# Performance work log

Measured on AMD Instinct MI355X. Metric: run time of the kernel, lower is better.

The kernel has to match this reference:

```python
import jax, jax.numpy as jnp
import numpy as np

B, N, D = 4, 2048, 1024
H, S, C, NSH, MV = 8, 3, 32, 3, 4


def _lin(key, fan_in, fan_out):
    k1, k2 = jax.random.split(key)
    lim = 1.0 / np.sqrt(fan_in)
    W = jax.random.uniform(k1, (fan_in, fan_out), minval=-lim, maxval=lim)
    b = jax.random.uniform(k2, (fan_out,), minval=-lim, maxval=lim)
    return W, b


def setup_inputs() -> dict:
    key = jax.random.key(0)
    ks = jax.random.split(key, 16)
    x = jax.random.normal(ks[0], (B, N, D), dtype=jnp.float32)
    W_sense, b_sense = _lin(ks[1], D, S * D)
    W_ctx, b_ctx = _lin(ks[2], D, D)
    W_sel, b_sel = _lin(ks[3], 2 * D, S)
    W_charge, b_charge = _lin(ks[4], D, 1)
    W_shell, b_shell = _lin(ks[5], D, NSH)
    W_class, b_class = _lin(ks[6], D, C)
    W_mass, b_mass = _lin(ks[7], D, 1)
    W_val, b_val = _lin(ks[8], D, MV)
    sparsity = 0.4
    init_val = -np.log(1.0 / sparsity - 1.0)
    compat_logits = jax.random.normal(ks[9], (C, C)) * 0.5 + init_val
    W_v, b_v = _lin(ks[10], D, D)
    W_out, b_out = _lin(ks[11], D, D)
    return {
        'x': x,
        'W_sense': W_sense, 'b_sense': b_sense,
        'W_ctx': W_ctx, 'b_ctx': b_ctx,
        'W_sel': W_sel, 'b_sel': b_sel,
        'W_charge': W_charge, 'b_charge': b_charge,
        'W_shell': W_shell, 'b_shell': b_shell,
        'W_class': W_class, 'b_class': b_class,
        'W_mass': W_mass, 'b_mass': b_mass,
        'W_val': W_val, 'b_val': b_val,
        'compat_logits': compat_logits.astype(jnp.float32),
        'w_charge': jnp.float32(1.0), 'w_shell': jnp.float32(0.5),
        'w_distance': jnp.float32(1.0), 'w_mass': jnp.float32(0.3),
        'w_valence': jnp.float32(0.3), 'temperature': jnp.float32(1.0),
        'W_v': W_v, 'b_v': b_v,
        'W_out': W_out, 'b_out': b_out,
    }


def reference(x, W_sense, b_sense, W_ctx, b_ctx, W_sel, b_sel,
              W_charge, b_charge, W_shell, b_shell, W_class, b_class,
              W_mass, b_mass, W_val, b_val, compat_logits,
              w_charge, w_shell, w_distance, w_mass, w_valence, temperature,
              W_v, b_v, W_out, b_out):
    b, n, d = x.shape
    sp = jax.nn.softplus

    # --- isotope selection (word-sense mixing) ---
    senses = (x @ W_sense + b_sense).reshape(b, n, S, d)          # (B,N,S,D)
    ctx_avg = (x @ W_ctx + b_ctx).mean(axis=1, keepdims=True)     # (B,1,D)
    sel_in = jnp.concatenate([x, jnp.broadcast_to(ctx_avg, (b, n, d))], axis=-1)
    sense_w = jax.nn.softmax(sel_in @ W_sel + b_sel, axis=-1)     # (B,N,S)
    x = jnp.einsum('bns,bnsd->bnd', sense_w, senses)

    # --- atomic properties ---
    charge = jnp.tanh(x @ W_charge + b_charge)[..., 0]            # (B,N)
    shell = jax.nn.softmax(x @ W_shell + b_shell, axis=-1)        # (B,N,NSH)
    cls = jnp.argmax(x @ W_class + b_class, axis=-1)              # (B,N) int
    mass = sp(x @ W_mass + b_mass)[..., 0] + 0.5                  # (B,N)
    val = jax.nn.softmax(x @ W_val + b_val, axis=-1)              # (B,N,MV)

    # --- class compatibility mask (B,N,N) ---
    compat = jax.nn.sigmoid((compat_logits + compat_logits.T) * 0.5)
    sparse_mask = compat[cls[:, :, None], cls[:, None, :]]

    # --- pairwise physics energy (B,N,N) ---
    pos = jnp.arange(n, dtype=x.dtype)
    dist = jnp.abs(pos[:, None] - pos[None, :])                   # (N,N)
    val_sum = val.sum(axis=-1)                                    # (B,N)
    E = (sp(w_charge) * charge[:, :, None] * charge[:, None, :]
         + sp(w_shell) * jnp.abs(shell[:, :, None, :] - shell[:, None, :, :]).sum(-1)
         - sp(w_distance) / (1.0 + 0.1 * dist)
         + sp(w_mass) * 0.1 * mass[:, :, None] * mass[:, None, :]
         - sp(w_valence) * (val_sum[:, :, None] + val_sum[:, None, :]) * 0.5)

    temp = sp(temperature)
    scores = (-E / temp) * sparse_mask
    causal = jnp.triu(jnp.ones((n, n), dtype=bool), k=1)
    scores = jnp.where(causal[None], -jnp.inf, scores)
    attn = jax.nn.softmax(scores, axis=-1)                        # (B,N,N)

    # --- weighted value aggregation (shared attn across heads) ---
    V = (x @ W_v + b_v).reshape(b, n, H, d // H)
    out = jnp.einsum('bij,bjhd->bihd', attn, V).reshape(b, n, d)
    return out @ W_out + b_out
```

## Files before the change

kernel.cpp:

```cpp
#include <hip/hip_runtime.h>
#include <hip/hip_bf16.h>
#include <cmath>

typedef __hip_bfloat16 bf16;
typedef __attribute__((ext_vector_type(4))) float floatx4;
typedef __attribute__((ext_vector_type(8))) short short8;
typedef __attribute__((ext_vector_type(8))) unsigned short ushort8;

__device__ __forceinline__ float bf2f(bf16 v) { return __bfloat162float(v); }
__device__ __forceinline__ bf16 f2bf(float v) { return __float2bfloat16(v); }
__device__ __forceinline__ float bfu2f(unsigned short u) { return __uint_as_float(((unsigned)u) << 16); }
__device__ __forceinline__ unsigned short f2bfu(float v) {
  bf16 h = __float2bfloat16(v);
  return __builtin_bit_cast(unsigned short, h);
}
__device__ __forceinline__ float softplusf(float x) {
  return x > 20.0f ? x : log1pf(expf(x));
}

__device__ __forceinline__ void async16(const void* g, void* l) {
  __builtin_amdgcn_global_load_lds(
      (const __attribute__((address_space(1))) unsigned int*)g,
      (__attribute__((address_space(3))) unsigned int*)l, 16, 0, 0);
}

template<int MODE, int CAUSAL, int ACCUM, int SWZ, int KSPLIT = 1>
__global__ __launch_bounds__(256) void gemm_bt(
    const bf16* __restrict__ A, const bf16* __restrict__ Bt,
    const float* __restrict__ bias, void* __restrict__ Cptr,
    int M, int N, int K, int lda, int ldb, int ldc,
    long aoffz, long boffz, long coffz)
{
  __shared__ __align__(16) bf16 As[128 * 32];
  __shared__ __align__(16) bf16 Bs[128 * 32];

  const int tid = threadIdx.x;
  const int lane = tid & 63;
  const int wave = tid >> 6;
  const int wr = wave >> 1, wc = wave & 1;
  const long z = blockIdx.z;
  int kstart = 0;
  long zz = z;
  if (KSPLIT > 1) {
    kstart = (int)(z % KSPLIT) * K;
    zz = z / KSPLIT;
  }
  A += zz * aoffz;
  Bt += zz * boffz;

  int bx, by;
  if (SWZ) {
    const int mtiles = M >> 7;
    const int per = mtiles >> 3;
    const int bid = (int)blockIdx.x;
    const int xcd = bid & 7;
    const int slot = bid >> 3;
    by = xcd * per + (slot % per);
    bx = slot / per;
  } else {
    bx = blockIdx.x;
    by = blockIdx.y;
  }
  const int m0 = by * 128, n0 = bx * 128;
  int kend = kstart + K;
  if (CAUSAL) {
    int klim = (by + 1) * 128;
    if (klim < kend) kend = klim;
  }

  floatx4 acc[4][4] = {};

  const int c0 = tid, c1 = tid + 256;
  const int ar0 = c0 >> 2, ak0 = (c0 & 3) * 8;
  const int ar1 = c1 >> 2, ak1 = (c1 & 3) * 8;
  const int fm = lane & 15, fk = (lane >> 4) * 8;

  for (int k0 = kstart; k0 < kend; k0 += 32) {
    async16(&A[(size_t)(m0 + ar0) * lda + k0 + ak0], &As[c0 * 8]);
    async16(&A[(size_t)(m0 + ar1) * lda + k0 + ak1], &As[c1 * 8]);
    async16(&Bt[(size_t)(n0 + ar0) * ldb + k0 + ak0], &Bs[c0 * 8]);
    async16(&Bt[(size_t)(n0 + ar1) * ldb + k0 + ak1], &Bs[c1 * 8]);
    __syncthreads();

    short8 af[4], bfr[4];
#pragma unroll
    for (int i = 0; i < 4; i++)
      af[i] = *(const short8*)&As[(wr * 64 + i * 16 + fm) * 32 + fk];
#pragma unroll
    for (int j = 0; j < 4; j++)
      bfr[j] = *(const short8*)&Bs[(wc * 64 + j * 16 + fm) * 32 + fk];
#pragma unroll
    for (int i = 0; i < 4; i++)
#pragma unroll
      for (int j = 0; j < 4; j++)
        acc[i][j] = __builtin_amdgcn_mfma_f32_16x16x32_bf16(af[i], bfr[j], acc[i][j], 0, 0, 0);
    __syncthreads();
  }

  const int rm0 = (lane >> 4) * 4, cn = lane & 15;
#pragma unroll
  for (int i = 0; i < 4; i++) {
#pragma unroll
    for (int j = 0; j < 4; j++) {
      int nn = n0 + wc * 64 + j * 16 + cn;
      float bv = bias ? bias[nn] : 0.0f;
#pragma unroll
      for (int r = 0; r < 4; r++) {
        int mm = m0 + wr * 64 + i * 16 + rm0 + r;
        float v = acc[i][j][r] + bv;
        if (MODE == 0) {
          ((bf16*)Cptr)[z * coffz + (long)mm * ldc + nn] = f2bf(v);
        } else if (MODE == 1) {
          long idx = z * coffz + (long)mm * ldc + nn;
          float* Cf = (float*)Cptr;
          if (ACCUM) v += Cf[idx];
          Cf[idx] = v;
        } else {
          long idx = ((long)((mm >> 11) * 1024 + nn)) * 2048 + (mm & 2047);
          ((bf16*)Cptr)[idx] = f2bf(v);
        }
      }
    }
  }
}

__global__ __launch_bounds__(256) void gemm_sense(
    const bf16* __restrict__ A, const bf16* __restrict__ Bt,
    const float* __restrict__ bias, const float* __restrict__ sw,
    bf16* __restrict__ y)
{
  __shared__ __align__(16) bf16 As[128 * 32];
  __shared__ __align__(16) bf16 Bs[128 * 32];

  const int tid = threadIdx.x;
  const int lane = tid & 63;
  const int wave = tid >> 6;
  const int wr = wave >> 1, wc = wave & 1;

  const int bid = (int)blockIdx.x;
  const int xcd = bid & 7;
  const int slot = bid >> 3;
  const int by = xcd * 8 + (slot & 7);
  const int bx = slot >> 3;
  const int m0 = by * 128, n0 = bx * 128;

  const int c0 = tid, c1 = tid + 256;
  const int ar0 = c0 >> 2, ak0 = (c0 & 3) * 8;
  const int ar1 = c1 >> 2, ak1 = (c1 & 3) * 8;
  const int fm = lane & 15, fk = (lane >> 4) * 8;
  const int rm0 = (lane >> 4) * 4, cn = lane & 15;

  floatx4 yacc[4][4] = {};

#pragma unroll 1
  for (int s = 0; s < 3; s++) {
    floatx4 acc[4][4] = {};
    const bf16* Bsrc = Bt + (size_t)(s * 1024 + n0) * 1024;
    for (int k0 = 0; k0 < 1024; k0 += 32) {
      async16(&A[(size_t)(m0 + ar0) * 3072 + k0 + ak0], &As[c0 * 8]);
      async16(&A[(size_t)(m0 + ar1) * 3072 + k0 + ak1], &As[c1 * 8]);
      async16(&Bsrc[(size_t)ar0 * 1024 + k0 + ak0], &Bs[c0 * 8]);
      async16(&Bsrc[(size_t)ar1 * 1024 + k0 + ak1], &Bs[c1 * 8]);
      __syncthreads();

      short8 af[4], bfr[4];
#pragma unroll
      for (int i = 0; i < 4; i++)
        af[i] = *(const short8*)&As[(wr * 64 + i * 16 + fm) * 32 + fk];
#pragma unroll
      for (int j = 0; j < 4; j++)
        bfr[j] = *(const short8*)&Bs[(wc * 64 + j * 16 + fm) * 32 + fk];
#pragma unroll
      for (int i = 0; i < 4; i++)
#pragma unroll
        for (int j = 0; j < 4; j++)
          acc[i][j] = __builtin_amdgcn_mfma_f32_16x16x32_bf16(af[i], bfr[j], acc[i][j], 0, 0, 0);
      __syncthreads();
    }
    float swm[4][4];
#pragma unroll
    for (int i = 0; i < 4; i++)
#pragma unroll
      for (int r = 0; r < 4; r++)
        swm[i][r] = sw[(size_t)(m0 + wr * 64 + i * 16 + rm0 + r) * 4 + s];
#pragma unroll
    for (int j = 0; j < 4; j++) {
      int nn = n0 + wc * 64 + j * 16 + cn;
      float bv = bias[s * 1024 + nn];
#pragma unroll
      for (int i = 0; i < 4; i++)
#pragma unroll
        for (int r = 0; r < 4; r++)
          yacc[i][j][r] += swm[i][r] * (acc[i][j][r] + bv);
    }
  }

#pragma unroll
  for (int i = 0; i < 4; i++)
#pragma unroll
    for (int j = 0; j < 4; j++) {
      int nn = n0 + wc * 64 + j * 16 + cn;
#pragma unroll
      for (int r = 0; r < 4; r++) {
        int mm = m0 + wr * 64 + i * 16 + rm0 + r;
        y[(size_t)mm * 1024 + nn] = f2bf(yacc[i][j][r]);
      }
    }
}

__global__ __launch_bounds__(256) void k_split_x3(const float* __restrict__ x,
                                                  bf16* __restrict__ xhhl) {
  long id = (long)blockIdx.x * 256 + threadIdx.x;
  if (id >= 8388608L) return;
  long t = id >> 10;
  int d = (int)(id & 1023);
  float v = x[id];
  bf16 h = f2bf(v);
  bf16 l = f2bf(v - bf2f(h));
  bf16* row = xhhl + t * 3072;
  row[d] = h;
  row[1024 + d] = h;
  row[2048 + d] = l;
}

__global__ __launch_bounds__(256) void k_split_ws3(const float* __restrict__ Ws,
                                                   bf16* __restrict__ Wsn3) {
  long id = (long)blockIdx.x * 256 + threadIdx.x;
  if (id >= 3145728L) return;
  int row10 = (int)(id >> 10);
  int d = row10 / 3;
  int s = row10 - d * 3;
  int dp = (int)(id & 1023);
  float v = Ws[id];
  bf16 h = f2bf(v);
  bf16 l = f2bf(v - bf2f(h));
  bf16* row = Wsn3 + ((size_t)(s * 1024 + d)) * 3072;
  row[dp] = h;
  row[1024 + dp] = l;
  row[2048 + dp] = h;
}

__global__ __launch_bounds__(256) void k_trans_hl(const float* __restrict__ src,
                                                  bf16* __restrict__ dh,
                                                  int R, int C) {
  __shared__ float tile[32][33];
  int c0 = blockIdx.x * 32, r0 = blockIdx.y * 32;
  int tx = threadIdx.x & 31, ty = threadIdx.x >> 5;
  for (int rr = ty; rr < 32; rr += 8)
    tile[rr][tx] = src[(size_t)(r0 + rr) * C + c0 + tx];
  __syncthreads();
  for (int rr = ty; rr < 32; rr += 8)
    dh[(size_t)(c0 + rr) * R + r0 + tx] = f2bf(tile[tx][rr]);
}

__global__ __launch_bounds__(256) void k_pack(
    const float* __restrict__ W_charge, const float* __restrict__ W_shell,
    const float* __restrict__ W_class, const float* __restrict__ W_mass,
    const float* __restrict__ b_charge, const float* __restrict__ b_shell,
    const float* __restrict__ b_class, const float* __restrict__ b_mass,
    const float* __restrict__ compat_logits,
    bf16* __restrict__ Whhl3, float* __restrict__ bhead, float* __restrict__ csig)
{
  int c = blockIdx.x;
  int tid = threadIdx.x;
  for (int e = tid; e < 1024; e += 256) {
    float v;
    if (c == 0) v = W_charge[e];
    else if (c < 4) v = W_shell[e * 3 + (c - 1)];
    else if (c == 4) v = W_mass[e];
    else if (c < 37) v = W_class[e * 32 + (c - 5)];
    else v = 0.0f;
    bf16 h = f2bf(v);
    bf16 l = f2bf(v - bf2f(h));
    bf16* row = Whhl3 + (size_t)c * 3072;
    row[e] = h;
    row[1024 + e] = h;
    row[2048 + e] = l;
  }
  if (c == 0 && tid < 37) {
    float v;
    if (tid == 0) v = b_charge[0];
    else if (tid < 4) v = b_shell[tid - 1];
    else if (tid == 4) v = b_mass[0];
    else v = b_class[tid - 5];
    bhead[tid] = v;
  }
  if (c == 1) {
    for (int k = tid; k < 1024; k += 256) {
      int ii = k >> 5, jj = k & 31;
      float l = 0.5f * (compat_logits[ii * 32 + jj] + compat_logits[jj * 32 + ii]);
      csig[k] = 1.0f / (1.0f + expf(-l));
    }
  }
}

__global__ __launch_bounds__(256) void k_bh(
    const float* __restrict__ b_sense, const float* __restrict__ W_charge,
    const float* __restrict__ W_shell, const float* __restrict__ W_class,
    const float* __restrict__ W_mass, float* __restrict__ bh)
{
  const int c = blockIdx.x, s = blockIdx.y;
  const int tid = threadIdx.x;
  __shared__ float red[256];
  float p = 0.0f;
  for (int e = tid; e < 1024; e += 256) {
    float w;
    if (c == 0) w = W_charge[e];
    else if (c < 4) w = W_shell[e * 3 + (c - 1)];
    else if (c == 4) w = W_mass[e];
    else w = W_class[e * 32 + (c - 5)];
    p += b_sense[s * 1024 + e] * w;
  }
  red[tid] = p;
  __syncthreads();
  for (int st = 128; st > 0; st >>= 1) {
    if (tid < st) red[tid] += red[tid + st];
    __syncthreads();
  }
  if (tid == 0) bh[s * 128 + c] = red[0];
}

__global__ __launch_bounds__(256) void k_reduce_mt(const float* __restrict__ Mtp,
                                                   float* __restrict__ Mt) {
  long o = (long)blockIdx.x * 256 + threadIdx.x;
  if (o >= 393216L) return;
  long s = o >> 17;
  long i = o & 131071;
  const float* p = Mtp + s * 8 * 131072 + i;
  float acc = 0.0f;
#pragma unroll
  for (int kc = 0; kc < 8; kc++) acc += p[(size_t)kc * 131072];
  Mt[o] = acc;
}

__global__ __launch_bounds__(256) void k_split(const float* __restrict__ Mt,
                                               const float* __restrict__ W_sel,
                                               bf16* __restrict__ Mthl) {
  long id = (long)blockIdx.x * 256 + threadIdx.x;
  if (id >= 1572864L) return;
  int n = (int)(id / 3072);
  int k = (int)(id - (long)n * 3072);
  int third = k >> 10;
  int j = k & 1023;
  float v;
  if (n < 384) {
    v = Mt[(size_t)n * 1024 + j];
  } else {
    int c2 = n - 384;
    v = (c2 < 3) ? W_sel[(size_t)j * 3 + c2] : 0.0f;
  }
  bf16 h = f2bf(v);
  Mthl[id] = (third == 1) ? f2bf(v - bf2f(h)) : h;
}

__global__ __launch_bounds__(256) void k_xbar(const float* __restrict__ x, float* __restrict__ xbar) {
  const int d = blockIdx.x * 256 + threadIdx.x;
  const int b = blockIdx.y;
  const int n0 = blockIdx.z * 256;
  const float* xb = x + (size_t)b * 2048 * 1024 + (size_t)n0 * 1024 + d;
  float s = 0.0f;
  for (int n = 0; n < 256; n++) s += xb[(size_t)n * 1024];
  atomicAdd(&xbar[b * 1024 + d], s * (1.0f / 2048.0f));
}

__global__ __launch_bounds__(256) void k_q(const float* __restrict__ W_ctx,
                                           const float* __restrict__ b_ctx,
                                           const float* __restrict__ W_sel,
                                           float* __restrict__ q) {
  const int e = blockIdx.x;
  const int tid = threadIdx.x;
  const float* row = (e < 1024) ? (W_ctx + (size_t)e * 1024) : b_ctx;
  float p0 = 0.0f, p1 = 0.0f, p2 = 0.0f;
  for (int d = tid; d < 1024; d += 256) {
    float v = row[d];
    const float* ws = W_sel + (size_t)(1024 + d) * 3;
    p0 += v * ws[0]; p1 += v * ws[1]; p2 += v * ws[2];
  }
  __shared__ float red[3][256];
  red[0][tid] = p0; red[1][tid] = p1; red[2][tid] = p2;
  __syncthreads();
  for (int st = 128; st > 0; st >>= 1) {
    if (tid < st) {
      red[0][tid] += red[0][tid + st];
      red[1][tid] += red[1][tid + st];
      red[2][tid] += red[2][tid + st];
    }
    __syncthreads();
  }
  if (tid < 3) q[(size_t)e * 3 + tid] = red[tid][0];
}

__global__ __launch_bounds__(256) void k_ctxsel(const float* __restrict__ xbar,
                                                const float* __restrict__ q,
                                                float* __restrict__ ctx_sel) {
  const int b = blockIdx.x;
  const int tid = threadIdx.x;
  float p0 = 0.0f, p1 = 0.0f, p2 = 0.0f;
  for (int e = tid; e < 1024; e += 256) {
    float v = xbar[b * 1024 + e];
    p0 += v * q[e * 3 + 0]; p1 += v * q[e * 3 + 1]; p2 += v * q[e * 3 + 2];
  }
  __shared__ float red[3][256];
  red[0][tid] = p0; red[1][tid] = p1; red[2][tid] = p2;
  __syncthreads();
  for (int st = 128; st > 0; st >>= 1) {
    if (tid < st) {
      red[0][tid] += red[0][tid + st];
      red[1][tid] += red[1][tid + st];
      red[2][tid] += red[2][tid + st];
    }
    __syncthreads();
  }
  if (tid < 3) ctx_sel[b * 3 + tid] = red[tid][0] + q[1024 * 3 + tid];
}

__global__ __launch_bounds__(64) void k_heads(
    const float* __restrict__ H, const float* __restrict__ ctx_sel,
    const float* __restrict__ b_sel, const float* __restrict__ bh,
    const float* __restrict__ bhead,
    float* __restrict__ sw, float* __restrict__ feat)
{
  const int t = blockIdx.x;
  const int b = t >> 11;
  const int lane = threadIdx.x;
  const float* Ht = H + (size_t)t * 512;
  const float* Ht2 = H + 4194304 + (size_t)t * 512;

  float s0 = Ht[384] + Ht2[384] + ctx_sel[b * 3 + 0] + b_sel[0];
  float s1 = Ht[385] + Ht2[385] + ctx_sel[b * 3 + 1] + b_sel[1];
  float s2 = Ht[386] + Ht2[386] + ctx_sel[b * 3 + 2] + b_sel[2];
  float mx = fmaxf(s0, fmaxf(s1, s2));
  float e0 = expf(s0 - mx), e1 = expf(s1 - mx), e2 = expf(s2 - mx);
  float inv = 1.0f / (e0 + e1 + e2);
  float w0 = e0 * inv, w1 = e1 * inv, w2 = e2 * inv;

  __shared__ float L[64];
  if (lane < 37) {
    float lg = bhead[lane];
    lg += w0 * (Ht[lane] + Ht2[lane] + bh[lane]);
    lg += w1 * (Ht[128 + lane] + Ht2[128 + lane] + bh[128 + lane]);
    lg += w2 * (Ht[256 + lane] + Ht2[256 + lane] + bh[256 + lane]);
    L[lane] = lg;
  }
  __syncthreads();
  if (lane == 0) {
    float charge = tanhf(L[0]);
    float h0 = L[1], h1 = L[2], h2 = L[3];
    float hm = fmaxf(h0, fmaxf(h1, h2));
    float x0 = expf(h0 - hm), x1 = expf(h1 - hm), x2 = expf(h2 - hm);
    float hinv = 1.0f / (x0 + x1 + x2);
    float mass = softplusf(L[4]) + 0.5f;
    int cls = 0;
    float best = L[5];
    for (int c = 1; c < 32; c++) {
      if (L[5 + c] > best) { best = L[5 + c]; cls = c; }
    }
    float* f = feat + (size_t)t * 8;
    f[0] = charge; f[1] = mass;
    f[2] = x0 * hinv; f[3] = x1 * hinv; f[4] = x2 * hinv;
    f[5] = (float)cls; f[6] = 0.0f; f[7] = 0.0f;
    float* sp_ = sw + (size_t)t * 4;
    sp_[0] = w0; sp_[1] = w1; sp_[2] = w2; sp_[3] = 0.0f;
  }
}

__global__ __launch_bounds__(256) void k_scores(
    const float* __restrict__ feat, const float* __restrict__ compat,
    const float* __restrict__ wchg, const float* __restrict__ wsh,
    const float* __restrict__ wdist, const float* __restrict__ wmass,
    const float* __restrict__ wval, const float* __restrict__ temp_p,
    bf16* __restrict__ P)
{
  const int i = blockIdx.x, b = blockIdx.y;
  const int tid = threadIdx.x;
  __shared__ float cs[1024];
  __shared__ float red[256];
  for (int k = tid; k < 1024; k += 256) cs[k] = compat[k];
  __syncthreads();

  const float a = softplusf(wchg[0]);
  const float bs = softplusf(wsh[0]);
  const float c = softplusf(wdist[0]);
  const float dm = softplusf(wmass[0]);
  const float ev = softplusf(wval[0]);
  const float itmp = 1.0f / softplusf(temp_p[0]);

  const float4* fi4 = (const float4*)(feat + ((size_t)b * 2048 + i) * 8);
  float4 fiA = fi4[0], fiB = fi4[1];
  const float ci = fiA.x, mi = fiA.y, si0 = fiA.z, si1 = fiA.w, si2 = fiB.x;
  int cli = (int)fiB.y; cli = cli < 0 ? 0 : (cli > 31 ? 31 : cli);

  float sc[8];
  float lmax = -3.0e38f;
#pragma unroll
  for (int jj = 0; jj < 8; jj++) {
    int j = tid + jj * 256;
    const float4* fj4 = (const float4*)(feat + ((size_t)b * 2048 + j) * 8);
    float4 fjA = fj4[0], fjB = fj4[1];
    int clj = (int)fjB.y; clj = clj < 0 ? 0 : (clj > 31 ? 31 : clj);
    float E = a * ci * fjA.x
            + bs * (fabsf(si0 - fjA.z) + fabsf(si1 - fjA.w) + fabsf(si2 - fjB.x))
            - c / (1.0f + 0.1f * fabsf((float)(i - j)))
            + dm * 0.1f * mi * fjA.y
            - ev;
    float s = (j <= i) ? (-E * itmp) * cs[cli * 32 + clj] : -3.0e38f;
    sc[jj] = s;
    lmax = fmaxf(lmax, s);
  }
  red[tid] = lmax;
  __syncthreads();
  for (int st = 128; st > 0; st >>= 1) {
    if (tid < st) red[tid] = fmaxf(red[tid], red[tid + st]);
    __syncthreads();
  }
  const float mrow = red[0];
  __syncthreads();

  float pv[8];
  float lsum = 0.0f;
#pragma unroll
  for (int jj = 0; jj < 8; jj++) {
    pv[jj] = (sc[jj] > -1.0e37f) ? expf(sc[jj] - mrow) : 0.0f;
    lsum += pv[jj];
  }
  red[tid] = lsum;
  __syncthreads();
  for (int st = 128; st > 0; st >>= 1) {
    if (tid < st) red[tid] += red[tid + st];
    __syncthreads();
  }
  const float inv = 1.0f / red[0];
  bf16* Pi = P + ((size_t)b * 2048 + i) * 2048;
#pragma unroll
  for (int jj = 0; jj < 8; jj++) Pi[tid + jj * 256] = f2bf(pv[jj] * inv);
}

extern "C" void kernel_launch(void* const* d_in, const int* in_sizes, int n_in,
                              void* d_out, int out_size, void* d_ws, size_t ws_size,
                              hipStream_t stream) {
  (void)in_sizes; (void)n_in; (void)out_size; (void)ws_size;
  const float* x        = (const float*)d_in[0];
  const float* W_sense  = (const float*)d_in[1];
  const float* b_sense  = (const float*)d_in[2];
  const float* W_ctx    = (const float*)d_in[3];
  const float* b_ctx    = (const float*)d_in[4];
  const float* W_sel    = (const float*)d_in[5];
  const float* b_sel    = (const float*)d_in[6];
  const float* W_charge = (const float*)d_in[7];
  const float* b_charge = (const float*)d_in[8];
  const float* W_shell  = (const float*)d_in[9];
  const float* b_shell  = (const float*)d_in[10];
  const float* W_class  = (const float*)d_in[11];
  const float* b_class  = (const float*)d_in[12];
  const float* W_mass   = (const float*)d_in[13];
  const float* b_mass   = (const float*)d_in[14];
  const float* compat_logits = (const float*)d_in[17];
  const float* w_charge = (const float*)d_in[18];
  const float* w_shell  = (const float*)d_in[19];
  const float* w_distance = (const float*)d_in[20];
  const float* w_mass   = (const float*)d_in[21];
  const float* w_valence = (const float*)d_in[22];
  const float* temperature = (const float*)d_in[23];
  const float* W_v      = (const float*)d_in[24];
  const float* b_v      = (const float*)d_in[25];
  const float* W_out    = (const float*)d_in[26];
  const float* b_out    = (const float*)d_in[27];

  char* w = (char*)d_ws;
  auto alloc = [&](size_t bytes) {
    char* p = w;
    w += (bytes + 255) & ~(size_t)255;
    return p;
  };
  bf16* xhhl  = (bf16*)alloc(8192ULL * 3072 * 2);
  char* R1    = alloc(48ULL * 1024 * 1024);
  bf16* Wsn3  = (bf16*)R1;
  float* Hh   = (float*)R1;
  float* Mtp  = (float*)(R1 + 20ULL * 1024 * 1024);
  bf16* Mthl  = (bf16*)(R1 + 40ULL * 1024 * 1024);
  float* Mt   = (float*)(R1 + 44ULL * 1024 * 1024);
  bf16* y     = (bf16*)R1;
  bf16* Wts_hi = (bf16*)alloc(3072ULL * 1024 * 2);
  bf16* Wt_v  = (bf16*)alloc(1024ULL * 1024 * 2);
  bf16* Wt_out = (bf16*)alloc(1024ULL * 1024 * 2);
  bf16* Whhl3 = (bf16*)alloc(128ULL * 3072 * 2);
  float* bh   = (float*)alloc(3ULL * 128 * 4);
  float* bhead = (float*)alloc(256);
  float* csig = (float*)alloc(4096);
  float* xbar = (float*)alloc(4ULL * 1024 * 4);
  float* qbuf = (float*)alloc(1025ULL * 3 * 4);
  float* ctx_sel = (float*)alloc(256);
  float* feat = (float*)alloc(8192ULL * 8 * 4);
  float* sw   = (float*)alloc(8192ULL * 4 * 4);
  bf16* Vt = xhhl + 8388608;
  bf16* O  = xhhl + 16777216;
  bf16* P  = (bf16*)d_out;

  k_split_x3<<<32768, 256, 0, stream>>>(x, xhhl);
  k_split_ws3<<<12288, 256, 0, stream>>>(W_sense, Wsn3);
  k_trans_hl<<<dim3(96, 32), 256, 0, stream>>>(W_sense, Wts_hi, 1024, 3072);
  k_trans_hl<<<dim3(32, 32), 256, 0, stream>>>(W_v, Wt_v, 1024, 1024);
  k_trans_hl<<<dim3(32, 32), 256, 0, stream>>>(W_out, Wt_out, 1024, 1024);
  k_pack<<<128, 256, 0, stream>>>(W_charge, W_shell, W_class, W_mass,
                                  b_charge, b_shell, b_class, b_mass,
                                  compat_logits, Whhl3, bhead, csig);

  hipMemsetAsync(xbar, 0, 4096 * 4, stream);
  k_xbar<<<dim3(4, 4, 8), 256, 0, stream>>>(x, xbar);
  k_q<<<1025, 256, 0, stream>>>(W_ctx, b_ctx, W_sel, qbuf);
  k_ctxsel<<<4, 256, 0, stream>>>(xbar, qbuf, ctx_sel);

  gemm_bt<1, 0, 0, 0, 8><<<dim3(8, 1, 24), 256, 0, stream>>>(
      Whhl3, Wsn3, nullptr, Mtp, 128, 1024, 384, 3072, 3072, 1024,
      0, 3145728L, 131072L);
  k_reduce_mt<<<1536, 256, 0, stream>>>(Mtp, Mt);
  k_split<<<6144, 256, 0, stream>>>(Mt, W_sel, Mthl);

  gemm_bt<1, 0, 0, 1, 2><<<dim3(256, 1, 2), 256, 0, stream>>>(
      xhhl, Mthl, nullptr, Hh, 8192, 512, 1536, 3072, 3072, 512,
      0, 0, 4194304L);

  k_bh<<<dim3(37, 3), 256, 0, stream>>>(b_sense, W_charge, W_shell, W_class, W_mass, bh);
  k_heads<<<8192, 64, 0, stream>>>(Hh, ctx_sel, b_sel, bh, bhead, sw, feat);

  gemm_sense<<<512, 256, 0, stream>>>(xhhl, Wts_hi, b_sense, sw, y);

  gemm_bt<2, 0, 0, 1><<<512, 256, 0, stream>>>(
      y, Wt_v, b_v, Vt, 8192, 1024, 1024, 1024, 1024, 0, 0, 0, 0);

  k_scores<<<dim3(2048, 4), 256, 0, stream>>>(feat, csig, w_charge, w_shell,
                                              w_distance, w_mass, w_valence, temperature, P);

  gemm_bt<0, 1, 0, 0><<<dim3(8, 16, 4), 256, 0, stream>>>(
      P, Vt, nullptr, O, 2048, 1024, 2048, 2048, 2048, 1024,
      2048L * 2048, 1024L * 2048, 2048L * 1024);

  gemm_bt<1, 0, 0, 1><<<512, 256, 0, stream>>>(
      O, Wt_out, b_out, (float*)d_out, 8192, 1024, 1024, 1024, 1024, 1024, 0, 0, 0);
}
```

Measured before the change: 601.7 us.

## Fold sense weights into prescaled A and double-buffer swizzled GEMM tiles

The sense-mixing GEMM is reformulated by prescaling x with each token's sense weights into a concatenated K=3072 operand, so a single GEMM with a K-concatenated transposed W_sense produces y directly, with the bias mix applied in the epilogue. This removes the three separate accumulation passes and per-pass epilogue work. All GEMMs also move to 64-wide K tiles with double-buffered LDS and an XOR swizzle, overlapping global loads with MFMA and cutting bank conflicts. The cost is an extra prescale kernel, double the LDS per block (which may lower occupancy), and bf16 rounding of the product s*x before the matmul rather than after.

```diff
diff --git a/kernel.cpp b/kernel.cpp
--- a/kernel.cpp
+++ b/kernel.cpp
@@ -31,8 +31,8 @@
     int M, int N, int K, int lda, int ldb, int ldc,
     long aoffz, long boffz, long coffz)
 {
-  __shared__ __align__(16) bf16 As[128 * 32];
-  __shared__ __align__(16) bf16 Bs[128 * 32];
+  __shared__ __align__(16) bf16 As[2][128 * 64];
+  __shared__ __align__(16) bf16 Bs[2][128 * 64];
 
   const int tid = threadIdx.x;
   const int lane = tid & 63;
@@ -68,33 +68,62 @@
     if (klim < kend) kend = klim;
   }
 
+  int aoff[4], boff[4];
+#pragma unroll
+  for (int q = 0; q < 4; q++) {
+    int ch = tid + 256 * q;
+    int r = ch >> 3, c4 = ch & 7;
+    int scol = (c4 ^ (r & 7)) * 8;
+    aoff[q] = (m0 + r) * lda + scol;
+    boff[q] = (n0 + r) * ldb + scol;
+  }
+
   floatx4 acc[4][4] = {};
-
-  const int c0 = tid, c1 = tid + 256;
-  const int ar0 = c0 >> 2, ak0 = (c0 & 3) * 8;
-  const int ar1 = c1 >> 2, ak1 = (c1 & 3) * 8;
-  const int fm = lane & 15, fk = (lane >> 4) * 8;
-
-  for (int k0 = kstart; k0 < kend; k0 += 32) {
-    async16(&A[(size_t)(m0 + ar0) * lda + k0 + ak0], &As[c0 * 8]);
-    async16(&A[(size_t)(m0 + ar1) * lda + k0 + ak1], &As[c1 * 8]);
-    async16(&Bt[(size_t)(n0 + ar0) * ldb + k0 + ak0], &Bs[c0 * 8]);
-    async16(&Bt[(size_t)(n0 + ar1) * ldb + k0 + ak1], &Bs[c1 * 8]);
+  const int fm = lane & 15, fq = lane >> 4;
+
+  const int nt = (kend - kstart) >> 6;
+
+#pragma unroll
+  for (int q = 0; q < 4; q++) {
+    int ch8 = (tid + 256 * q) * 8;
+    async16(&A[(size_t)aoff[q] + kstart], &As[0][ch8]);
+    async16(&Bt[(size_t)boff[q] + kstart], &Bs[0][ch8]);
+  }
+  __syncthreads();
+
+  int cur = 0;
+  for (int t = 0; t < nt; t++) {
+    if (t + 1 < nt) {
+      const int k0 = kstart + (t + 1) * 64;
+#pragma unroll
+      for (int q = 0; q < 4; q++) {
+        int ch8 = (tid + 256 * q) * 8;
+        async16(&A[(size_t)aoff[q] + k0], &As[cur ^ 1][ch8]);
+        async16(&Bt[(size_t)boff[q] + k0], &Bs[cur ^ 1][ch8]);
+      }
+    }
+#pragma unroll
+    for (int kk = 0; kk < 2; kk++) {
+      short8 af[4], bfr[4];
+      const int c4 = fq + 4 * kk;
+#pragma unroll
+      for (int i = 0; i < 4; i++) {
+        int R = wr * 64 + i * 16 + fm;
+        af[i] = *(const short8*)&As[cur][(R * 8 + (c4 ^ (R & 7))) * 8];
+      }
+#pragma unroll
+      for (int j = 0; j < 4; j++) {
+        int R = wc * 64 + j * 16 + fm;
+        bfr[j] = *(const short8*)&Bs[cur][(R * 8 + (c4 ^ (R & 7))) * 8];
+      }
+#pragma unroll
+      for (int i = 0; i < 4; i++)
+#pragma unroll
+        for (int j = 0; j < 4; j++)
+          acc[i][j] = __builtin_amdgcn_mfma_f32_16x16x32_bf16(af[i], bfr[j], acc[i][j], 0, 0, 0);
+    }
     __syncthreads();
-
-    short8 af[4], bfr[4];
-#pragma unroll
-    for (int i = 0; i < 4; i++)
-      af[i] = *(const short8*)&As[(wr * 64 + i * 16 + fm) * 32 + fk];
-#pragma unroll
-    for (int j = 0; j < 4; j++)
-      bfr[j] = *(const short8*)&Bs[(wc * 64 + j * 16 + fm) * 32 + fk];
-#pragma unroll
-    for (int i = 0; i < 4; i++)
-#pragma unroll
-      for (int j = 0; j < 4; j++)
-        acc[i][j] = __builtin_amdgcn_mfma_f32_16x16x32_bf16(af[i], bfr[j], acc[i][j], 0, 0, 0);
-    __syncthreads();
+    cur ^= 1;
   }
 
   const int rm0 = (lane >> 4) * 4, cn = lane & 15;
@@ -124,13 +153,13 @@
   }
 }
 
-__global__ __launch_bounds__(256) void gemm_sense(
+__global__ __launch_bounds__(256) void gemm_y(
     const bf16* __restrict__ A, const bf16* __restrict__ Bt,
-    const float* __restrict__ bias, const float* __restrict__ sw,
+    const float* __restrict__ bsense, const float* __restrict__ sw,
     bf16* __restrict__ y)
 {
-  __shared__ __align__(16) bf16 As[128 * 32];
-  __shared__ __align__(16) bf16 Bs[128 * 32];
+  __shared__ __align__(16) bf16 As[2][128 * 64];
+  __shared__ __align__(16) bf16 Bs[2][128 * 64];
 
   const int tid = threadIdx.x;
   const int lane = tid & 63;
@@ -144,68 +173,103 @@
   const int bx = slot >> 3;
   const int m0 = by * 128, n0 = bx * 128;
 
-  const int c0 = tid, c1 = tid + 256;
-  const int ar0 = c0 >> 2, ak0 = (c0 & 3) * 8;
-  const int ar1 = c1 >> 2, ak1 = (c1 & 3) * 8;
-  const int fm = lane & 15, fk = (lane >> 4) * 8;
-  const int rm0 = (lane >> 4) * 4, cn = lane & 15;
-
-  floatx4 yacc[4][4] = {};
-
-#pragma unroll 1
-  for (int s = 0; s < 3; s++) {
-    floatx4 acc[4][4] = {};
-    const bf16* Bsrc = Bt + (size_t)(s * 1024 + n0) * 1024;
-    for (int k0 = 0; k0 < 1024; k0 += 32) {
-      async16(&A[(size_t)(m0 + ar0) * 3072 + k0 + ak0], &As[c0 * 8]);
-      async16(&A[(size_t)(m0 + ar1) * 3072 + k0 + ak1], &As[c1 * 8]);
-      async16(&Bsrc[(size_t)ar0 * 1024 + k0 + ak0], &Bs[c0 * 8]);
-      async16(&Bsrc[(size_t)ar1 * 1024 + k0 + ak1], &Bs[c1 * 8]);
-      __syncthreads();
-
+  int aoff[4], boff[4];
+#pragma unroll
+  for (int q = 0; q < 4; q++) {
+    int ch = tid + 256 * q;
+    int r = ch >> 3, c4 = ch & 7;
+    int scol = (c4 ^ (r & 7)) * 8;
+    aoff[q] = (m0 + r) * 3072 + scol;
+    boff[q] = (n0 + r) * 3072 + scol;
+  }
+
+  floatx4 acc[4][4] = {};
+  const int fm = lane & 15, fq = lane >> 4;
+
+#pragma unroll
+  for (int q = 0; q < 4; q++) {
+    int ch8 = (tid + 256 * q) * 8;
+    async16(&A[(size_t)aoff[q]], &As[0][ch8]);
+    async16(&Bt[(size_t)boff[q]], &Bs[0][ch8]);
+  }
+  __syncthreads();
+
+  int cur = 0;
+  for (int t = 0; t < 48; t++) {
+    if (t + 1 < 48) {
+      const int k0 = (t + 1) * 64;
+#pragma unroll
+      for (int q = 0; q < 4; q++) {
+        int ch8 = (tid + 256 * q) * 8;
+        async16(&A[(size_t)aoff[q] + k0], &As[cur ^ 1][ch8]);
+        async16(&Bt[(size_t)boff[q] + k0], &Bs[cur ^ 1][ch8]);
+      }
+    }
+#pragma unroll
+    for (int kk = 0; kk < 2; kk++) {
       short8 af[4], bfr[4];
-#pragma unroll
-      for (int i = 0; i < 4; i++)
-        af[i] = *(const short8*)&As[(wr * 64 + i * 16 + fm) * 32 + fk];
-#pragma unroll
-      for (int j = 0; j < 4; j++)
-        bfr[j] = *(const short8*)&Bs[(wc * 64 + j * 16 + fm) * 32 + fk];
+      const int c4 = fq + 4 * kk;
+#pragma unroll
+      for (int i = 0; i < 4; i++) {
+        int R = wr * 64 + i * 16 + fm;
+        af[i] = *(const short8*)&As[cur][(R * 8 + (c4 ^ (R & 7))) * 8];
+      }
+#pragma unroll
+      for (int j = 0; j < 4; j++) {
+        int R = wc * 64 + j * 16 + fm;
+        bfr[j] = *(const short8*)&Bs[cur][(R * 8 + (c4 ^ (R & 7))) * 8];
+      }
 #pragma unroll
       for (int i = 0; i < 4; i++)
 #pragma unroll
         for (int j = 0; j < 4; j++)
           acc[i][j] = __builtin_amdgcn_mfma_f32_16x16x32_bf16(af[i], bfr[j], acc[i][j], 0, 0, 0);
-      __syncthreads();
-    }
-    float swm[4][4];
-#pragma unroll
-    for (int i = 0; i < 4; i++)
-#pragma unroll
-      for (int r = 0; r < 4; r++)
-        swm[i][r] = sw[(size_t)(m0 + wr * 64 + i * 16 + rm0 + r) * 4 + s];
-#pragma unroll
-    for (int j = 0; j < 4; j++) {
-      int nn = n0 + wc * 64 + j * 16 + cn;
-      float bv = bias[s * 1024 + nn];
-#pragma unroll
-      for (int i = 0; i < 4; i++)
-#pragma unroll
-        for (int r = 0; r < 4; r++)
-          yacc[i][j][r] += swm[i][r] * (acc[i][j][r] + bv);
-    }
-  }
-
-#pragma unroll
-  for (int i = 0; i < 4; i++)
-#pragma unroll
-    for (int j = 0; j < 4; j++) {
-      int nn = n0 + wc * 64 + j * 16 + cn;
+    }
+    __syncthreads();
+    cur ^= 1;
+  }
+
+  const int rm0 = (lane >> 4) * 4, cn = lane & 15;
+#pragma unroll
+  for (int j = 0; j < 4; j++) {
+    int nn = n0 + wc * 64 + j * 16 + cn;
+    float b0 = bsense[nn], b1 = bsense[1024 + nn], b2 = bsense[2048 + nn];
+#pragma unroll
+    for (int i = 0; i < 4; i++) {
 #pragma unroll
       for (int r = 0; r < 4; r++) {
         int mm = m0 + wr * 64 + i * 16 + rm0 + r;
-        y[(size_t)mm * 1024 + nn] = f2bf(yacc[i][j][r]);
+        const float* sm = sw + (size_t)mm * 4;
+        float v = acc[i][j][r] + sm[0] * b0 + sm[1] * b1 + sm[2] * b2;
+        y[(size_t)mm * 1024 + nn] = f2bf(v);
       }
     }
+  }
+}
+
+__global__ __launch_bounds__(256) void k_prescale(const float* __restrict__ x,
+                                                  const float* __restrict__ sw,
+                                                  bf16* __restrict__ Ap) {
+  long id = (long)blockIdx.x * 256 + threadIdx.x;
+  if (id >= 1048576L) return;
+  int t = (int)(id >> 7);
+  int kc = (int)(id & 127) << 3;
+  const float* xt = x + (size_t)t * 1024 + kc;
+  float4 a = *(const float4*)xt;
+  float4 b = *(const float4*)(xt + 4);
+  const float s0 = sw[t * 4 + 0], s1 = sw[t * 4 + 1], s2 = sw[t * 4 + 2];
+  float v[8] = {a.x, a.y, a.z, a.w, b.x, b.y, b.z, b.w};
+  ushort8 o0, o1, o2;
+#pragma unroll
+  for (int e = 0; e < 8; e++) {
+    o0[e] = f2bfu(s0 * v[e]);
+    o1[e] = f2bfu(s1 * v[e]);
+    o2[e] = f2bfu(s2 * v[e]);
+  }
+  bf16* row = Ap + (size_t)t * 3072 + kc;
+  *(ushort8*)(row) = o0;
+  *(ushort8*)(row + 1024) = o1;
+  *(ushort8*)(row + 2048) = o2;
 }
 
 __global__ __launch_bounds__(256) void k_split_x3(const float* __restrict__ x,
@@ -251,6 +315,18 @@
   __syncthreads();
   for (int rr = ty; rr < 32; rr += 8)
     dh[(size_t)(c0 + rr) * R + r0 + tx] = f2bf(tile[tx][rr]);
+}
+
+__global__ __launch_bounds__(256) void k_trans_sense(const float* __restrict__ Ws,
+                                                     bf16* __restrict__ Bt2) {
+  __shared__ float tile[32][33];
+  int c0 = blockIdx.x * 32, r0 = blockIdx.y * 32, s = blockIdx.z;
+  int tx = threadIdx.x & 31, ty = threadIdx.x >> 5;
+  for (int rr = ty; rr < 32; rr += 8)
+    tile[rr][tx] = Ws[(size_t)(r0 + rr) * 3072 + s * 1024 + c0 + tx];
+  __syncthreads();
+  for (int rr = ty; rr < 32; rr += 8)
+    Bt2[(size_t)(c0 + rr) * 3072 + s * 1024 + r0 + tx] = f2bf(tile[tx][rr]);
 }
 
 __global__ __launch_bounds__(256) void k_pack(
@@ -580,7 +656,7 @@
   bf16* Mthl  = (bf16*)(R1 + 40ULL * 1024 * 1024);
   float* Mt   = (float*)(R1 + 44ULL * 1024 * 1024);
   bf16* y     = (bf16*)R1;
-  bf16* Wts_hi = (bf16*)alloc(3072ULL * 1024 * 2);
+  bf16* Wts2  = (bf16*)alloc(3072ULL * 1024 * 2);
   bf16* Wt_v  = (bf16*)alloc(1024ULL * 1024 * 2);
   bf16* Wt_out = (bf16*)alloc(1024ULL * 1024 * 2);
   bf16* Whhl3 = (bf16*)alloc(128ULL * 3072 * 2);
@@ -592,13 +668,14 @@
   float* ctx_sel = (float*)alloc(256);
   float* feat = (float*)alloc(8192ULL * 8 * 4);
   float* sw   = (float*)alloc(8192ULL * 4 * 4);
+  bf16* Aprime = xhhl;
   bf16* Vt = xhhl + 8388608;
   bf16* O  = xhhl + 16777216;
   bf16* P  = (bf16*)d_out;
 
   k_split_x3<<<32768, 256, 0, stream>>>(x, xhhl);
   k_split_ws3<<<12288, 256, 0, stream>>>(W_sense, Wsn3);
-  k_trans_hl<<<dim3(96, 32), 256, 0, stream>>>(W_sense, Wts_hi, 1024, 3072);
+  k_trans_sense<<<dim3(32, 32, 3), 256, 0, stream>>>(W_sense, Wts2);
   k_trans_hl<<<dim3(32, 32), 256, 0, stream>>>(W_v, Wt_v, 1024, 1024);
   k_trans_hl<<<dim3(32, 32), 256, 0, stream>>>(W_out, Wt_out, 1024, 1024);
   k_pack<<<128, 256, 0, stream>>>(W_charge, W_shell, W_class, W_mass,
@@ -623,7 +700,9 @@
   k_bh<<<dim3(37, 3), 256, 0, stream>>>(b_sense, W_charge, W_shell, W_class, W_mass, bh);
   k_heads<<<8192, 64, 0, stream>>>(Hh, ctx_sel, b_sel, bh, bhead, sw, feat);
 
-  gemm_sense<<<512, 256, 0, stream>>>(xhhl, Wts_hi, b_sense, sw, y);
+  k_prescale<<<4096, 256, 0, stream>>>(x, sw, Aprime);
+
+  gemm_y<<<512, 256, 0, stream>>>(Aprime, Wts2, b_sense, sw, y);
 
   gemm_bt<2, 0, 0, 1><<<512, 256, 0, stream>>>(
       y, Wt_v, b_v, Vt, 8192, 1024, 1024, 1024, 1024, 0, 0, 0, 0);
```

Result: faster. 546.3 us (-9.2%).
